# Performance work log

Measured on AMD Instinct MI355X. Metric: run time of the kernel, lower is better.

## Reference

```python
import jax, jax.numpy as jnp
import numpy as np

B, L, D = 2, 2048, 2048
H, KVH, HD, FD = 8, 1, 256, 64   # heads, kv heads, head_dim, feature_dim
CHUNK = 64


def setup_inputs() -> dict:
    key = jax.random.key(0)
    ks = jax.random.split(key, 8)
    hidden_states = jax.random.normal(ks[0], (B, L, D), dtype=jnp.float32)
    # Gemma-style RoPE tables over half the head dim
    half = HD // 2
    inv_freq = 1.0 / (10000.0 ** (jnp.arange(half, dtype=jnp.float32) / half))
    ang = jnp.arange(L, dtype=jnp.float32)[:, None] * inv_freq[None, :]  # [L, half]
    freqs_cos, freqs_sin = jnp.cos(ang), jnp.sin(ang)
    mask = jnp.ones((1, 1, L, L), dtype=bool)  # unused in linear path
    s = 0.02
    Wq = jax.random.normal(ks[1], (D, H * HD), dtype=jnp.float32) * s
    Wk = jax.random.normal(ks[2], (D, KVH * HD), dtype=jnp.float32) * s
    Wv = jax.random.normal(ks[3], (D, KVH * HD), dtype=jnp.float32) * s
    Wo = jax.random.normal(ks[4], (H * HD, D), dtype=jnp.float32) * s
    fmq = jax.random.normal(ks[5], (H, HD, FD), dtype=jnp.float32) * s
    fmk = jax.random.normal(ks[6], (H, HD, FD), dtype=jnp.float32) * s
    return dict(hidden_states=hidden_states, freqs_cos=freqs_cos, freqs_sin=freqs_sin,
                mask=mask, Wq=Wq, Wk=Wk, Wv=Wv, Wo=Wo, fmq=fmq, fmk=fmk)


def _rope(x, cos, sin):
    # x: [B, L, h, HD]; Gemma complex RoPE: first half = real, second half = imag
    half = x.shape[-1] // 2
    x1, x2 = x[..., :half], x[..., half:]
    c = cos[None, :, None, :]
    s = sin[None, :, None, :]
    return jnp.concatenate([x1 * c - x2 * s, x1 * s + x2 * c], axis=-1)


def _hedgehog(x, W):
    # x: [B, H, L, HD], W: [H, HD, FD] -> softmax over cat([xW, -xW]) -> [B,H,L,2*FD]
    p = jnp.einsum('bhld,hdf->bhlf', x, W)
    return jax.nn.softmax(jnp.concatenate([p, -p], axis=-1), axis=-1)


def _chunk_linear_attn(q, k, v, chunk=CHUNK):
    # q,k: [B,H,L,F]; v: [B,H,L,HD]; chunked causal linear attention
    b, h, l, f = q.shape
    dv = v.shape[-1]
    n = l // chunk
    q = q.reshape(b, h, n, chunk, f) * (f ** -0.5)
    k = k.reshape(b, h, n, chunk, f)
    v = v.reshape(b, h, n, chunk, dv)
    kv = jnp.einsum('bhncf,bhncd->bhnfd', k, v)            # per-chunk KV
    kv = jnp.cumsum(kv, axis=2)
    kv = jnp.concatenate([jnp.zeros_like(kv[:, :, :1]), kv[:, :, :-1]], axis=2)  # exclusive prefix
    inter = jnp.einsum('bhncf,bhnfd->bhncd', q, kv)        # cross-chunk term
    s = jnp.einsum('bhnif,bhnjf->bhnij', q, k)             # intra-chunk scores
    tri = jnp.tril(jnp.ones((chunk, chunk), dtype=bool))
    s = jnp.where(tri, s, 0.0)
    intra = jnp.einsum('bhnij,bhnjd->bhnid', s, v)
    return (inter + intra).reshape(b, h, l, dv)


def reference(hidden_states, freqs_cos, freqs_sin, mask, Wq, Wk, Wv, Wo, fmq, fmk):
    b, l, _ = hidden_states.shape
    q = (hidden_states @ Wq).reshape(b, l, H, HD)
    k = (hidden_states @ Wk).reshape(b, l, KVH, HD)
    v = (hidden_states @ Wv).reshape(b, l, KVH, HD)
    q = _rope(q, freqs_cos, freqs_sin)
    k = _rope(k, freqs_cos, freqs_sin)
    # repeat_interleave kv heads to num_heads (MQA expansion)
    rep = H // KVH
    k = jnp.repeat(k, rep, axis=2)
    v = jnp.repeat(v, rep, axis=2)
    q = jnp.transpose(q, (0, 2, 1, 3))  # [B,H,L,HD]
    k = jnp.transpose(k, (0, 2, 1, 3))
    v = jnp.transpose(v, (0, 2, 1, 3))
    q = _hedgehog(q, fmq)
    k = _hedgehog(k, fmk)
    o = _chunk_linear_attn(q, k, v)                         # [B,H,L,HD]
    o = jnp.transpose(o, (0, 2, 1, 3)).reshape(b, l, H * HD)
    return o @ Wo
```

## Files before the change

kernel.cpp:

```cpp
#include <hip/hip_runtime.h>

#define B_ 2
#define L_ 2048
#define D_ 2048
#define H_ 8
#define HD_ 256
#define FD_ 64
#define F_ 128
#define NC_ 32
#define M_ (B_*L_)
#define SCALE_Q 0.08838834764831845f

typedef unsigned short u16;
typedef __attribute__((ext_vector_type(8))) short bf16x8;
typedef __attribute__((ext_vector_type(8))) unsigned short u16x8;
typedef __attribute__((ext_vector_type(4))) unsigned short u16x4;
typedef __attribute__((ext_vector_type(16))) float f32x16;
typedef __attribute__((ext_vector_type(4))) unsigned int u32x4;

#define FMA4(a_, s_, v_) { (a_).x += (s_)*(v_).x; (a_).y += (s_)*(v_).y; \
                           (a_).z += (s_)*(v_).z; (a_).w += (s_)*(v_).w; }


__device__ __forceinline__ u16 bf16_rne(float x) {
  unsigned u = __float_as_uint(x);
  return (u16)((u + 0x7fffu + ((u >> 16) & 1u)) >> 16);
}
__device__ __forceinline__ void bf16_split(float x, u16& h, u16& l) {
  unsigned u = __float_as_uint(x);
  unsigned hb = (u + 0x7fffu + ((u >> 16) & 1u)) >> 16;
  h = (u16)hb;
  float hf = __uint_as_float(hb << 16);
  l = bf16_rne(x - hf);
}

__device__ __forceinline__ void gl_lds16(const u16* g, u16* l) {
  __builtin_amdgcn_global_load_lds(
      (const __attribute__((address_space(1))) unsigned int*)g,
      (__attribute__((address_space(3))) unsigned int*)l, 16, 0, 0);
}

__device__ __forceinline__ size_t kvb_off(int d, int f) {
  return (size_t)(((d >> 7) & 1) * 16384 + ((f >> 5) & 3) * 4096 +
                  ((d >> 6) & 1) * 2048 + ((f >> 4) & 1) * 1024 +
                  ((d >> 5) & 1) * 512 + ((f >> 3) & 1) * 256 +
                  (d & 31) * 8 + (f & 7));
}
__device__ __forceinline__ size_t vb_off(int d, int j) {
  return (size_t)(((d >> 7) & 1) * 8192 + ((j >> 5) & 1) * 4096 +
                  ((d >> 6) & 1) * 2048 + ((j >> 4) & 1) * 1024 +
                  ((d >> 5) & 1) * 512 + ((j >> 3) & 1) * 256 +
                  (d & 31) * 8 + (j & 7));
}

__device__ __forceinline__ void wtrans_body(const float* __restrict__ W, int Nsrc,
                                            int n0, u16* __restrict__ dst,
                                            int P, int kt) {
  int t = threadIdx.x;
  int nn = t & 127, kh = t >> 7;
  const float* src = W + (size_t)(kt * 32 + kh * 16) * Nsrc + n0 + nn;
  u16x8 u0, u1;
  #pragma unroll
  for (int kk = 0; kk < 8; ++kk) u0[kk] = bf16_rne(src[(size_t)kk * Nsrc]);
  #pragma unroll
  for (int kk = 0; kk < 8; ++kk) u1[kk] = bf16_rne(src[(size_t)(kk + 8) * Nsrc]);
  size_t base = ((size_t)P * 64 + kt) * 4096 + (size_t)((nn >> 6) & 1) * 2048
              + (size_t)kh * 1024 + (size_t)((nn >> 5) & 1) * 512
              + (size_t)(nn & 31) * 8;
  *(u16x8*)(dst + base) = u0;
  *(u16x8*)(dst + base + 256) = u1;
}

__global__ __launch_bounds__(256)
void prep_kernel(const float* __restrict__ hs,
                 const float* __restrict__ Wq, const float* __restrict__ Wk,
                 const float* __restrict__ Wv, const float* __restrict__ Wo,
                 const float* __restrict__ fmq, const float* __restrict__ fmk,
                 u16* __restrict__ hsHt, u16* __restrict__ hsLt,
                 u16* __restrict__ WTh, u16* __restrict__ WoTh,
                 u16* __restrict__ fmbtH, u16* __restrict__ fmbtL) {
  int bid = blockIdx.x;
  if (bid < 4096) {
    int gid = bid * 256 + threadIdx.x;
    int r = gid >> 8, u = gid & 255;
    const float* src = hs + (size_t)r * 2048 + u * 8;
    float4 v0 = *(const float4*)src, v1 = *(const float4*)(src + 4);
    float vals[8] = {v0.x, v0.y, v0.z, v0.w, v1.x, v1.y, v1.z, v1.w};
    u16x8 hv, lv;
    #pragma unroll
    for (int j = 0; j < 8; ++j) { u16 hh, ll; bf16_split(vals[j], hh, ll); hv[j] = hh; lv[j] = ll; }
    size_t off = ((size_t)(r >> 6) * 64 + (u >> 2)) * 2048
               + (size_t)((u >> 1) & 1) * 1024 + (size_t)((r >> 5) & 1) * 512
               + (size_t)(u & 1) * 256 + (size_t)(r & 31) * 8;
    *(u16x8*)(hsHt + off) = hv;
    *(u16x8*)(hsLt + off) = lv;
  } else if (bid < 5376) {
    int idx = bid - 4096;
    int P = idx >> 6, kt = idx & 63;
    const float* W; int Nsrc, n0;
    if (P < 16)      { W = Wq; Nsrc = 2048; n0 = P * 128; }
    else if (P < 18) { W = Wk; Nsrc = 256;  n0 = (P - 16) * 128; }
    else             { W = Wv; Nsrc = 256;  n0 = (P - 18) * 128; }
    wtrans_body(W, Nsrc, n0, WTh, P, kt);
  } else if (bid < 5504) {
    int idx = bid - 5376;
    int h16 = idx >> 3, kt = idx & 7;
    const float* src = (h16 < 8) ? (fmq + (size_t)h16 * 16384)
                                 : (fmk + (size_t)(h16 - 8) * 16384);
    int t = threadIdx.x;
    int f = t & 63, kq = t >> 6;
    u16x8 hv, lv;
    #pragma unroll
    for (int i = 0; i < 8; ++i) {
      float val = src[(size_t)(kt * 32 + kq * 8 + i) * 64 + f];
      u16 hh, ll; bf16_split(val, hh, ll); hv[i] = hh; lv[i] = ll;
    }
    size_t base = (size_t)(h16 * 8 + kt) * 2048 + (size_t)(kq >> 1) * 1024
                + (size_t)(f >> 5) * 512 + (size_t)(kq & 1) * 256
                + (size_t)(f & 31) * 8;
    *(u16x8*)(fmbtH + base) = hv;
    *(u16x8*)(fmbtL + base) = lv;
  } else {
    int idx = bid - 5504;
    wtrans_body(Wo, 2048, (idx >> 6) * 128, WoTh, idx >> 6, idx & 63);
  }
}

__global__ __launch_bounds__(256)
void wtrans_wo(const float* __restrict__ Wo, u16* __restrict__ WoTh) {
  wtrans_body(Wo, 2048, blockIdx.x * 128, WoTh, blockIdx.x, blockIdx.y);
}

__global__ __launch_bounds__(256)
void prep_v(const float* __restrict__ v, u16* __restrict__ vbH,
            u16* __restrict__ vbL) {
  int bn = blockIdx.x;
  const float* vp = v + (size_t)bn * 64 * HD_;
  size_t cbout = (size_t)bn * 16384;
  int d = threadIdx.x;
  #pragma unroll
  for (int it = 0; it < 8; ++it) {
    int j0 = it * 8;
    u16x8 hv, lv;
    #pragma unroll
    for (int c = 0; c < 8; ++c) {
      u16 hh, ll; bf16_split(vp[(size_t)(j0 + c) * HD_ + d], hh, ll);
      hv[c] = hh; lv[c] = ll;
    }
    size_t off = cbout + vb_off(d, j0);
    *(u16x8*)(vbH + off) = hv;
    *(u16x8*)(vbL + off) = lv;
  }
}

__device__ __forceinline__ void mfma_body(
    const u16* __restrict__ AtH, const u16* __restrict__ AtL,
    const u16* __restrict__ Bt, float* __restrict__ C, int cstride,
    int bm, int bn) {
  __shared__ __align__(16) u16 AsH[2048];
  __shared__ __align__(16) u16 AsL[2048];
  __shared__ __align__(16) u16 Bs[4096];
  const int t = threadIdx.x, lane = t & 63, wv = t >> 6;
  const u16* aSrc = (wv ? AtL : AtH) + (size_t)bm * 131072 + lane * 8;
  const u16* bSrc = Bt + (size_t)bn * 262144 + wv * 2048 + lane * 8;
  u16* aDst = wv ? AsL : AsH;
  u16* bDst = Bs + wv * 2048;

  f32x16 acc[2][2];
  #pragma unroll
  for (int a = 0; a < 2; ++a)
    #pragma unroll
    for (int b2 = 0; b2 < 2; ++b2)
      #pragma unroll
      for (int r = 0; r < 16; ++r) acc[a][b2][r] = 0.f;

  for (int kt = 0; kt < 64; ++kt) {
    const u16* ak = aSrc + (size_t)kt * 2048;
    const u16* bk = bSrc + (size_t)kt * 4096;
    __syncthreads();
    #pragma unroll
    for (int c = 0; c < 4; ++c) {
      gl_lds16(ak + c * 512, aDst + c * 512);
      gl_lds16(bk + c * 512, bDst + c * 512);
    }
    __syncthreads();

    #pragma unroll
    for (int ks = 0; ks < 2; ++ks) {
      const u16* ph = AsH + ks * 1024 + lane * 8;
      const u16* pl = AsL + ks * 1024 + lane * 8;
      const u16* pb = Bs + wv * 2048 + ks * 1024 + lane * 8;
      bf16x8 a0 = *(const bf16x8*)ph;
      bf16x8 a1 = *(const bf16x8*)(ph + 512);
      bf16x8 b0 = *(const bf16x8*)pb;
      bf16x8 b1 = *(const bf16x8*)(pb + 512);
      acc[0][0] = __builtin_amdgcn_mfma_f32_32x32x16_bf16(a0, b0, acc[0][0], 0, 0, 0);
      acc[0][1] = __builtin_amdgcn_mfma_f32_32x32x16_bf16(a0, b1, acc[0][1], 0, 0, 0);
      acc[1][0] = __builtin_amdgcn_mfma_f32_32x32x16_bf16(a1, b0, acc[1][0], 0, 0, 0);
      acc[1][1] = __builtin_amdgcn_mfma_f32_32x32x16_bf16(a1, b1, acc[1][1], 0, 0, 0);
      bf16x8 l0 = *(const bf16x8*)pl;
      bf16x8 l1 = *(const bf16x8*)(pl + 512);
      acc[0][0] = __builtin_amdgcn_mfma_f32_32x32x16_bf16(l0, b0, acc[0][0], 0, 0, 0);
      acc[0][1] = __builtin_amdgcn_mfma_f32_32x32x16_bf16(l0, b1, acc[0][1], 0, 0, 0);
      acc[1][0] = __builtin_amdgcn_mfma_f32_32x32x16_bf16(l1, b0, acc[1][0], 0, 0, 0);
      acc[1][1] = __builtin_amdgcn_mfma_f32_32x32x16_bf16(l1, b1, acc[1][1], 0, 0, 0);
    }
  }

  const int fr = lane & 31, g = lane >> 5;
  float* Cp = C + (size_t)(bm * 64) * cstride + wv * 64;
  #pragma unroll
  for (int mt = 0; mt < 2; ++mt)
    #pragma unroll
    for (int nt = 0; nt < 2; ++nt) {
      #pragma unroll
      for (int r = 0; r < 16; ++r) {
        int row = mt * 32 + (r & 3) + 8 * (r >> 2) + 4 * g;
        Cp[(size_t)row * cstride + nt * 32 + fr] = acc[mt][nt][r];
      }
    }
}

#define SUB_ 12288
#define MFB(a_, b_, c_) (c_) = __builtin_amdgcn_mfma_f32_32x32x16_bf16((a_), (b_), (c_), 0, 0, 0)

__device__ __forceinline__ void mfma_big_body(
    const u16* __restrict__ AtH, const u16* __restrict__ AtL,
    const u16* __restrict__ Bt, float* __restrict__ C, int cstride,
    int bm, int bn) {
  __shared__ __align__(16) u16 lds[3 * SUB_];
  const int t = threadIdx.x, lane = t & 63, wv = t >> 6;
  const int wm = wv >> 1, wn = wv & 1;

  const u16* gs[6];
  unsigned lo[6], gst[6];
  #pragma unroll
  for (int j = 0; j < 6; ++j) {
    int line = wv * 6 + j;
    if (line < 8) {
      gs[j] = AtH + ((size_t)(2 * bm + (line >> 2)) * 64) * 2048
                  + (size_t)(line & 3) * 512 + lane * 8;
      gst[j] = 2048;
    } else if (line < 16) {
      int l2 = line - 8;
      gs[j] = AtL + ((size_t)(2 * bm + (l2 >> 2)) * 64) * 2048
                  + (size_t)(l2 & 3) * 512 + lane * 8;
      gst[j] = 2048;
    } else {
      int l3 = line - 16;
      gs[j] = Bt + (size_t)bn * 262144 + (size_t)l3 * 512 + lane * 8;
      gst[j] = 4096;
    }
    lo[j] = line * 512;
  }

  f32x16 acc[2][2];
  #pragma unroll
  for (int a = 0; a < 2; ++a)
    #pragma unroll
    for (int b2 = 0; b2 < 2; ++b2)
      #pragma unroll
      for (int r = 0; r < 16; ++r) acc[a][b2][r] = 0.f;

  #pragma unroll
  for (int j = 0; j < 6; ++j) gl_lds16(gs[j], lds + lo[j]);
  #pragma unroll
  for (int j = 0; j < 6; ++j) gl_lds16(gs[j] + gst[j], lds + SUB_ + lo[j]);
  asm volatile("s_waitcnt vmcnt(6)" ::: "memory");
  __builtin_amdgcn_s_barrier();
  __builtin_amdgcn_sched_barrier(0);

  int cb = 0;
  for (int kt = 0; kt < 64; ++kt) {
    int sb = cb + 2 * SUB_; if (sb >= 3 * SUB_) sb -= 3 * SUB_;
    const u16* base = lds + cb;
    const u16* ph0 = base + wm * 2048 + lane * 8;
    const u16* pb0 = base + 8192 + wn * 2048 + lane * 8;

    bf16x8 a0 = *(const bf16x8*)(ph0);
    bf16x8 a1 = *(const bf16x8*)(ph0 + 512);
    bf16x8 l0 = *(const bf16x8*)(ph0 + 4096);
    bf16x8 l1 = *(const bf16x8*)(ph0 + 4608);
    bf16x8 b0 = *(const bf16x8*)(pb0);
    bf16x8 b1 = *(const bf16x8*)(pb0 + 512);
    if (kt < 62) {
      gl_lds16(gs[0] + (size_t)(kt + 2) * gst[0], lds + sb + lo[0]);
      gl_lds16(gs[1] + (size_t)(kt + 2) * gst[1], lds + sb + lo[1]);
      gl_lds16(gs[2] + (size_t)(kt + 2) * gst[2], lds + sb + lo[2]);
    }
    __builtin_amdgcn_s_barrier();
    asm volatile("s_waitcnt lgkmcnt(0)" ::: "memory");
    __builtin_amdgcn_sched_barrier(0);
    __builtin_amdgcn_s_setprio(1);
    MFB(a0, b0, acc[0][0]); MFB(a0, b1, acc[0][1]);
    MFB(a1, b0, acc[1][0]); MFB(a1, b1, acc[1][1]);
    MFB(l0, b0, acc[0][0]); MFB(l0, b1, acc[0][1]);
    MFB(l1, b0, acc[1][0]); MFB(l1, b1, acc[1][1]);
    __builtin_amdgcn_s_setprio(0);
    __builtin_amdgcn_s_barrier();
    __builtin_amdgcn_sched_barrier(0);

    bf16x8 c0 = *(const bf16x8*)(ph0 + 1024);
    bf16x8 c1 = *(const bf16x8*)(ph0 + 1536);
    bf16x8 m0 = *(const bf16x8*)(ph0 + 5120);
    bf16x8 m1 = *(const bf16x8*)(ph0 + 5632);
    bf16x8 d0 = *(const bf16x8*)(pb0 + 1024);
    bf16x8 d1 = *(const bf16x8*)(pb0 + 1536);
    if (kt < 62) {
      gl_lds16(gs[3] + (size_t)(kt + 2) * gst[3], lds + sb + lo[3]);
      gl_lds16(gs[4] + (size_t)(kt + 2) * gst[4], lds + sb + lo[4]);
      gl_lds16(gs[5] + (size_t)(kt + 2) * gst[5], lds + sb + lo[5]);
    }
    __builtin_amdgcn_s_barrier();
    asm volatile("s_waitcnt lgkmcnt(0)" ::: "memory");
    __builtin_amdgcn_sched_barrier(0);
    __builtin_amdgcn_s_setprio(1);
    MFB(c0, d0, acc[0][0]); MFB(c0, d1, acc[0][1]);
    MFB(c1, d0, acc[1][0]); MFB(c1, d1, acc[1][1]);
    MFB(m0, d0, acc[0][0]); MFB(m0, d1, acc[0][1]);
    MFB(m1, d0, acc[1][0]); MFB(m1, d1, acc[1][1]);
    __builtin_amdgcn_s_setprio(0);
    if (kt < 62) asm volatile("s_waitcnt vmcnt(6)" ::: "memory");
    else         asm volatile("s_waitcnt vmcnt(0)" ::: "memory");
    __builtin_amdgcn_s_barrier();
    __builtin_amdgcn_sched_barrier(0);
    cb += SUB_; if (cb == 3 * SUB_) cb = 0;
  }

  const int fr = lane & 31, g = lane >> 5;
  float* Cp = C + (size_t)(bm * 128 + wm * 64) * cstride + wn * 64;
  #pragma unroll
  for (int mt = 0; mt < 2; ++mt)
    #pragma unroll
    for (int nt = 0; nt < 2; ++nt) {
      #pragma unroll
      for (int r = 0; r < 16; ++r) {
        int row = mt * 32 + (r & 3) + 8 * (r >> 2) + 4 * g;
        Cp[(size_t)row * cstride + nt * 32 + fr] = acc[mt][nt][r];
      }
    }
}

__global__ __launch_bounds__(256, 2)
void mfma_q(const u16* __restrict__ hsHt, const u16* __restrict__ hsLt,
            const u16* __restrict__ WTh, float* __restrict__ q) {
  mfma_big_body(hsHt, hsLt, WTh, q + blockIdx.x * 128, 2048,
                blockIdx.y, blockIdx.x);
}

__global__ __launch_bounds__(128, 4)
void mfma_kv(const u16* __restrict__ hsHt, const u16* __restrict__ hsLt,
             const u16* __restrict__ WTh,
             float* __restrict__ k, float* __restrict__ v) {
  int bn = blockIdx.x;
  float* Cb; int co;
  if (bn < 2) { Cb = k; co = bn * 128; }
  else        { Cb = v; co = (bn - 2) * 128; }
  mfma_body(hsHt, hsLt, WTh, Cb + co, 256, blockIdx.y, 16 + bn);
}

__global__ __launch_bounds__(256, 2)
void mfma_wo(const u16* __restrict__ oHt, const u16* __restrict__ oLt,
             const u16* __restrict__ WoTh, float* __restrict__ out) {
  mfma_big_body(oHt, oLt, WoTh, out + blockIdx.x * 128, 2048,
                blockIdx.y, blockIdx.x);
}

__global__ __launch_bounds__(256, 1)
void mfma_hh(const float* __restrict__ q, const float* __restrict__ kx,
             const float* __restrict__ cosb, const float* __restrict__ sinb,
             const u16* __restrict__ fmbtH, const u16* __restrict__ fmbtL,
             float* __restrict__ qf, float* __restrict__ kf,
             const float* __restrict__ vsrc,
             u16* __restrict__ vbH, u16* __restrict__ vbL) {
  int bid = blockIdx.x;
  if (bid >= 512) {
    int bn = bid - 512;
    const float* vp = vsrc + (size_t)bn * 64 * HD_;
    size_t cbout = (size_t)bn * 16384;
    int d = threadIdx.x;
    #pragma unroll
    for (int it = 0; it < 8; ++it) {
      int j0 = it * 8;
      u16x8 hv, lv;
      #pragma unroll
      for (int c = 0; c < 8; ++c) {
        u16 hh, ll; bf16_split(vp[(size_t)(j0 + c) * HD_ + d], hh, ll);
        hv[c] = hh; lv[c] = ll;
      }
      size_t off = cbout + vb_off(d, j0);
      *(u16x8*)(vbH + off) = hv;
      *(u16x8*)(vbL + off) = lv;
    }
    return;
  }
  __shared__ __align__(16) u16 xlds[65536];
  const int t = threadIdx.x;
  const int rt = bid & 31, h16 = bid >> 5;
  const int rowbase = rt * 128;
  const float* xsrc; size_t xstr;
  if (h16 < 8) { xsrc = q + (size_t)h16 * 256; xstr = 2048; }
  else         { xsrc = kx;                    xstr = 256; }

  for (int iter = 0; iter < 16; ++iter) {
    int flat = iter * 1024 + t * 4;
    int r = flat >> 7, dd = flat & 127;
    int grow = rowbase + r;
    int l = grow & 2047;
    const float* xr = xsrc + (size_t)grow * xstr + dd;
    float4 x1 = *(const float4*)xr;
    float4 x2 = *(const float4*)(xr + 128);
    float4 c  = *(const float4*)(cosb + (size_t)l * 128 + dd);
    float4 s  = *(const float4*)(sinb + (size_t)l * 128 + dd);
    float lo4[4] = {x1.x*c.x - x2.x*s.x, x1.y*c.y - x2.y*s.y,
                    x1.z*c.z - x2.z*s.z, x1.w*c.w - x2.w*s.w};
    float hi4[4] = {x1.x*s.x + x2.x*c.x, x1.y*s.y + x2.y*c.y,
                    x1.z*s.z + x2.z*c.z, x1.w*s.w + x2.w*c.w};
    int rt32 = r >> 5, r5 = r & 31;
    #pragma unroll
    for (int half = 0; half < 2; ++half) {
      int d = dd + half * 128;
      int kt = d >> 5, k = d & 31;
      unsigned base = (unsigned)((kt * 4 + rt32) * 2) * 1024
                    + (unsigned)(k >> 4) * 512 + (unsigned)((k >> 3) & 1) * 256
                    + (unsigned)r5 * 8 + (unsigned)(k & 7);
      const float* vv = half ? hi4 : lo4;
      u16x4 hv, lv;
      #pragma unroll
      for (int j = 0; j < 4; ++j) {
        u16 hh, ll; bf16_split(vv[j], hh, ll); hv[j] = hh; lv[j] = ll;
      }
      *(u16x4*)(xlds + base) = hv;
      *(u16x4*)(xlds + 1024 + base) = lv;
    }
  }
  __syncthreads();

  const int w = t >> 6, lane = t & 63;
  f32x16 acc[2];
  #pragma unroll
  for (int nt = 0; nt < 2; ++nt)
    #pragma unroll
    for (int r = 0; r < 16; ++r) acc[nt][r] = 0.f;

  const u16* fmbH = fmbtH + (size_t)h16 * 8 * 2048;
  const u16* fmbL = fmbtL + (size_t)h16 * 8 * 2048;
  #pragma unroll
  for (int kt = 0; kt < 8; ++kt) {
    unsigned xb = (unsigned)((kt * 4 + w) * 2) * 1024;
    #pragma unroll
    for (int ks = 0; ks < 2; ++ks) {
      bf16x8 xh = *(const bf16x8*)(xlds + xb + ks * 512 + lane * 8);
      bf16x8 xl = *(const bf16x8*)(xlds + xb + 1024 + ks * 512 + lane * 8);
      #pragma unroll
      for (int nt = 0; nt < 2; ++nt) {
        size_t fb = (size_t)kt * 2048 + ks * 1024 + nt * 512 + lane * 8;
        bf16x8 bh_ = *(const bf16x8*)((const short*)(fmbH + fb));
        bf16x8 bl_ = *(const bf16x8*)((const short*)(fmbL + fb));
        MFB(xh, bh_, acc[nt]); MFB(xl, bh_, acc[nt]); MFB(xh, bl_, acc[nt]);
      }
    }
  }

  const int g = lane >> 5, f31 = lane & 31;
  float* outp = (h16 < 8) ? qf : kf;
  const int hh = h16 & 7;
  #pragma unroll
  for (int r = 0; r < 16; ++r) {
    int rowl = (r & 3) + 8 * (r >> 2) + 4 * g;
    int grow = rowbase + w * 32 + rowl;
    float p0 = acc[0][r], p1 = acc[1][r];
    float m = fmaxf(fabsf(p0), fabsf(p1));
    #pragma unroll
    for (int off = 16; off > 0; off >>= 1) m = fmaxf(m, __shfl_xor(m, off, 64));
    float e0 = __expf(p0 - m),  e0n = __expf(-p0 - m);
    float e1 = __expf(p1 - m),  e1n = __expf(-p1 - m);
    float zl = e0 + e0n + e1 + e1n;
    #pragma unroll
    for (int off = 16; off > 0; off >>= 1) zl += __shfl_xor(zl, off, 64);
    float inv = 1.0f / zl;
    int b = grow >> 11, l = grow & 2047;
    size_t ob = ((size_t)((b * 8 + hh) * 2048 + l)) * 128;
    outp[ob + f31]       = e0 * inv;
    outp[ob + 32 + f31]  = e1 * inv;
    outp[ob + 64 + f31]  = e0n * inv;
    outp[ob + 96 + f31]  = e1n * inv;
  }
}

__global__ __launch_bounds__(256)
void chunk_kv_kernel(const float* __restrict__ kf, const float* __restrict__ v,
                     u16* __restrict__ kvbH, u16* __restrict__ kvbL) {
  __shared__ __align__(16) float kfs[64][128];
  int n = blockIdx.x & (NC_ - 1), bh = blockIdx.x >> 5;
  int b = bh >> 3;
  const float* kfp = kf + ((size_t)bh * L_ + (size_t)n * 64) * F_;
  int t = threadIdx.x;
  #pragma unroll
  for (int it = 0; it < 8; ++it) {
    int flat = t * 4 + it * 1024;
    *(float4*)&kfs[flat >> 7][flat & 127] = *(const float4*)(kfp + flat);
  }
  __syncthreads();
  int dg = t & 63;
  int fg = t >> 6;
  const float* vp = v + (size_t)(b * L_ + n * 64) * HD_ + dg * 4;
  size_t cb = (size_t)blockIdx.x * 32768;
  #pragma unroll
  for (int pass = 0; pass < 4; ++pass) {
    int f0 = fg * 8 + pass * 32;
    float4 acc[8];
    #pragma unroll
    for (int i = 0; i < 8; ++i) acc[i] = make_float4(0.f, 0.f, 0.f, 0.f);
    for (int j = 0; j < 64; ++j) {
      float4 vv = *(const float4*)(vp + (size_t)j * HD_);
      float4 ka = *(const float4*)&kfs[j][f0];
      float4 kb = *(const float4*)&kfs[j][f0 + 4];
      FMA4(acc[0], ka.x, vv); FMA4(acc[1], ka.y, vv);
      FMA4(acc[2], ka.z, vv); FMA4(acc[3], ka.w, vv);
      FMA4(acc[4], kb.x, vv); FMA4(acc[5], kb.y, vv);
      FMA4(acc[6], kb.z, vv); FMA4(acc[7], kb.w, vv);
    }
    #pragma unroll
    for (int c = 0; c < 4; ++c) {
      u16x8 hv, lv;
      #pragma unroll
      for (int ff = 0; ff < 8; ++ff) {
        float xs = (c == 0) ? acc[ff].x : (c == 1) ? acc[ff].y
                 : (c == 2) ? acc[ff].z : acc[ff].w;
        u16 hh, ll; bf16_split(xs, hh, ll); hv[ff] = hh; lv[ff] = ll;
      }
      int d = dg * 4 + c;
      size_t off = cb + kvb_off(d, f0);
      *(u16x8*)(kvbH + off) = hv;
      *(u16x8*)(kvbL + off) = lv;
    }
  }
}

__global__ __launch_bounds__(256)
void chunk_scan_kernel(u16* __restrict__ kvbH, u16* __restrict__ kvbL) {
  int bh = blockIdx.x >> 4, g = blockIdx.x & 15;
  int d = threadIdx.x;
  size_t off = kvb_off(d, g * 8);
  float run[8] = {0.f, 0.f, 0.f, 0.f, 0.f, 0.f, 0.f, 0.f};
  for (int n = 0; n < NC_; ++n) {
    size_t a = ((size_t)(bh * 32 + n)) * 32768 + off;
    u16x8 hv = *(u16x8*)(kvbH + a);
    u16x8 lv = *(u16x8*)(kvbL + a);
    u16x8 oh, ol;
    #pragma unroll
    for (int c = 0; c < 8; ++c) {
      float val = __uint_as_float((unsigned)hv[c] << 16)
                + __uint_as_float((unsigned)lv[c] << 16);
      u16 hh, ll; bf16_split(run[c], hh, ll); oh[c] = hh; ol[c] = ll;
      run[c] += val;
    }
    *(u16x8*)(kvbH + a) = oh;
    *(u16x8*)(kvbL + a) = ol;
  }
}

__global__ __launch_bounds__(256, 2)
void chunk_attn_kernel(const float* __restrict__ qf, const float* __restrict__ kf,
                       const u16* __restrict__ vbH, const u16* __restrict__ vbL,
                       const u16* __restrict__ kvbH, const u16* __restrict__ kvbL,
                       u16* __restrict__ oHt, u16* __restrict__ oLt) {
  __shared__ __align__(16) u16 lds[32768];
  const int n = blockIdx.x & (NC_ - 1), bh = blockIdx.x >> 5;
  const int h = bh & 7, b = bh >> 3;
  const int t = threadIdx.x;
  const int w = t >> 6, i31 = t & 31, G = (t >> 5) & 1;
  const int l8 = (t & 63) * 8;

  {
    const float* qp = qf + ((size_t)bh * L_ + (size_t)n * 64) * F_;
    const float* kp = kf + ((size_t)bh * L_ + (size_t)n * 64) * F_;
    int o8 = t & 15, ib = t >> 4;
    #pragma unroll
    for (int iter = 0; iter < 4; ++iter) {
      int i = ib + iter * 16;
      int it = i >> 5, ks = o8 >> 1;
      int sub = (it * 8 + ks) * 512 + (o8 & 1) * 256 + (i & 31) * 8;
      {
        const float* src = qp + (size_t)i * 128 + o8 * 8;
        float4 a = *(const float4*)src, c = *(const float4*)(src + 4);
        float vals[8] = {a.x, a.y, a.z, a.w, c.x, c.y, c.z, c.w};
        u16x8 hv, lv;
        #pragma unroll
        for (int j = 0; j < 8; ++j) {
          u16 hh, ll; bf16_split(vals[j] * SCALE_Q, hh, ll);
          hv[j] = hh; lv[j] = ll;
        }
        *(u16x8*)(lds + sub) = hv;
        *(u16x8*)(lds + 8192 + sub) = lv;
      }
      {
        const float* src = kp + (size_t)i * 128 + o8 * 8;
        float4 a = *(const float4*)src, c = *(const float4*)(src + 4);
        float vals[8] = {a.x, a.y, a.z, a.w, c.x, c.y, c.z, c.w};
        u16x8 hv, lv;
        #pragma unroll
        for (int j = 0; j < 8; ++j) {
          u16 hh, ll; bf16_split(vals[j], hh, ll);
          hv[j] = hh; lv[j] = ll;
        }
        *(u16x8*)(lds + 16384 + sub) = hv;
        *(u16x8*)(lds + 24576 + sub) = lv;
      }
    }
  }
  __syncthreads();

  const u16* Lq  = lds;
  const u16* Lql = lds + 8192;
  const u16* Lk  = lds + 16384;
  const u16* Lkl = lds + 24576;

  f32x16 st[2][2];
  #pragma unroll
  for (int a = 0; a < 2; ++a)
    #pragma unroll
    for (int c = 0; c < 2; ++c)
      #pragma unroll
      for (int r = 0; r < 16; ++r) st[a][c][r] = 0.f;

  #pragma unroll
  for (int ks = 0; ks < 8; ++ks) {
    bf16x8 kh0 = *(const bf16x8*)(Lk  + ks * 512 + l8);
    bf16x8 kh1 = *(const bf16x8*)(Lk  + (8 + ks) * 512 + l8);
    bf16x8 kl0 = *(const bf16x8*)(Lkl + ks * 512 + l8);
    bf16x8 kl1 = *(const bf16x8*)(Lkl + (8 + ks) * 512 + l8);
    bf16x8 qh0 = *(const bf16x8*)(Lq  + ks * 512 + l8);
    bf16x8 qh1 = *(const bf16x8*)(Lq  + (8 + ks) * 512 + l8);
    bf16x8 ql0 = *(const bf16x8*)(Lql + ks * 512 + l8);
    bf16x8 ql1 = *(const bf16x8*)(Lql + (8 + ks) * 512 + l8);
    MFB(kh0, qh0, st[0][0]); MFB(kh0, ql0, st[0][0]); MFB(kl0, qh0, st[0][0]);
    MFB(kh0, qh1, st[0][1]); MFB(kh0, ql1, st[0][1]); MFB(kl0, qh1, st[0][1]);
    MFB(kh1, qh0, st[1][0]); MFB(kh1, ql0, st[1][0]); MFB(kl1, qh0, st[1][0]);
    MFB(kh1, qh1, st[1][1]); MFB(kh1, ql1, st[1][1]); MFB(kl1, qh1, st[1][1]);
  }

// ... 62 lines not shown

  {
    size_t cb = (size_t)blockIdx.x * 32768;
    #pragma unroll
    for (int ks = 0; ks < 8; ++ks) {
      bf16x8 qa_h0 = *(const bf16x8*)(Lq  + ks * 512 + l8);
      bf16x8 qa_h1 = *(const bf16x8*)(Lq  + (8 + ks) * 512 + l8);
      bf16x8 qa_l0 = *(const bf16x8*)(Lql + ks * 512 + l8);
      bf16x8 qa_l1 = *(const bf16x8*)(Lql + (8 + ks) * 512 + l8);
      #pragma unroll
      for (int nt = 0; nt < 2; ++nt) {
        size_t base = cb + kvb_off(w * 64 + nt * 32, ks * 16) + l8;
        bf16x8 kvH = *(const bf16x8*)((const short*)(kvbH + base));
        bf16x8 kvL = *(const bf16x8*)((const short*)(kvbL + base));
        MFB(qa_h0, kvH, acc[0][nt]); MFB(qa_l0, kvH, acc[0][nt]);
        MFB(qa_h0, kvL, acc[0][nt]);
        MFB(qa_h1, kvH, acc[1][nt]); MFB(qa_l1, kvH, acc[1][nt]);
        MFB(qa_h1, kvL, acc[1][nt]);
      }
    }
  }

  {
    int p = b * NC_ + n;
    #pragma unroll
    for (int mt = 0; mt < 2; ++mt)
      #pragma unroll
      for (int nt = 0; nt < 2; ++nt) {
        int u_ = h * 32 + w * 8 + nt * 4 + (i31 >> 3);
        size_t ob = ((size_t)p * 64 + (u_ >> 2)) * 2048
                  + (size_t)((u_ >> 1) & 1) * 1024 + (size_t)mt * 512
                  + (size_t)(u_ & 1) * 256 + (size_t)(i31 & 7);
        #pragma unroll
        for (int r = 0; r < 16; ++r) {
          int rr = (r & 3) + 8 * (r >> 2) + 4 * G;
          u16 hh, ll; bf16_split(acc[mt][nt][r], hh, ll);
          oHt[ob + (size_t)rr * 8] = hh;
          oLt[ob + (size_t)rr * 8] = ll;
        }
      }
  }
}

extern "C" void kernel_launch(void* const* d_in, const int* in_sizes, int n_in,
                              void* d_out, int out_size, void* d_ws, size_t ws_size,
                              hipStream_t stream) {
  const float* hs   = (const float*)d_in[0];
  const float* fcos = (const float*)d_in[1];
  const float* fsin = (const float*)d_in[2];
  const float* Wq  = (const float*)d_in[4];
  const float* Wk  = (const float*)d_in[5];
  const float* Wv  = (const float*)d_in[6];
  const float* Wo  = (const float*)d_in[7];
  const float* fmq = (const float*)d_in[8];
  const float* fmk = (const float*)d_in[9];
  float* out = (float*)d_out;

  float* ws = (float*)d_ws;
  float* q  = ws;
  float* k  = q  + (size_t)M_ * 2048;
  float* v  = k  + (size_t)M_ * 256;
  float* qf = v  + (size_t)M_ * 256;
  float* kf = qf + (size_t)B_ * H_ * L_ * F_;
  float* kvr = kf + (size_t)B_ * H_ * L_ * F_;

  u16* hsHt = (u16*)kvr;
  u16* hsLt = hsHt + (size_t)M_ * 2048;
  u16* WTh  = hsLt + (size_t)M_ * 2048;
  u16* fmbtH = WTh + (size_t)1280 * 4096;
  u16* fmbtL = fmbtH + (size_t)131072 * 2;
  u16* kvbH = (u16*)kvr;
  u16* kvbL = kvbH + (size_t)512 * 32768;
  u16* oHt  = (u16*)q;
  u16* oLt  = oHt + (size_t)M_ * 2048;

  const size_t WS_BASE = (size_t)142606336;
  bool bigws = ws_size >= WS_BASE + (size_t)12582912;
  u16* WoTh = bigws ? (u16*)((char*)d_ws + WS_BASE) : (u16*)kvr;
  u16* vbH  = bigws ? (u16*)((char*)d_ws + WS_BASE + 8388608) : (u16*)k;
  u16* vbL  = vbH + (size_t)64 * 16384;

  prep_kernel<<<bigws ? 6528 : 5504, 256, 0, stream>>>(
      hs, Wq, Wk, Wv, Wo, fmq, fmk, hsHt, hsLt, WTh, WoTh, fmbtH, fmbtL);
  mfma_q<<<dim3(16, 32), 256, 0, stream>>>(hsHt, hsLt, WTh, q);
  mfma_kv<<<dim3(4, 64), 128, 0, stream>>>(hsHt, hsLt, WTh, k, v);
  mfma_hh<<<bigws ? 576 : 512, 256, 0, stream>>>(
      q, k, fcos, fsin, fmbtH, fmbtL, qf, kf, v, vbH, vbL);
  if (!bigws)
    prep_v<<<B_ * NC_, 256, 0, stream>>>(v, vbH, vbL);
  chunk_kv_kernel<<<B_ * H_ * NC_, 256, 0, stream>>>(kf, v, kvbH, kvbL);
  chunk_scan_kernel<<<256, 256, 0, stream>>>(kvbH, kvbL);
  chunk_attn_kernel<<<B_ * H_ * NC_, 256, 0, stream>>>(qf, kf, vbH, vbL,
                                                       kvbH, kvbL, oHt, oLt);
  if (!bigws)
    wtrans_wo<<<dim3(16, 64), 256, 0, stream>>>(Wo, WoTh);
  mfma_wo<<<dim3(16, 32), 256, 0, stream>>>(oHt, oLt, WoTh, out);
}
```

Baseline: 481.2 us.

## Merge Q and KV projections into one launch and fuse chunk KV with scan

The separate Q and K/V projection GEMMs become a single mfma_qkv launch that uses the big 128x128 tile body for all 20 column blocks. The per-chunk KV outer-product kernel and the prefix-scan kernel are fused into one kernel that keeps a running KV sum in registers, so per-chunk KV partials are no longer written and read back. The cost is that the fused scan runs only 256 blocks sequentially over 32 chunks, doing scalar FMAs per thread, which cuts parallelism compared with the 512-block chunk_kv kernel.

Result: slower. 500.1 us (+3.9%).

```diff
diff --git a/kernel.cpp b/kernel.cpp
--- a/kernel.cpp
+++ b/kernel.cpp
@@ -17,9 +17,6 @@
 typedef __attribute__((ext_vector_type(4))) unsigned short u16x4;
 typedef __attribute__((ext_vector_type(16))) float f32x16;
 typedef __attribute__((ext_vector_type(4))) unsigned int u32x4;
-
-#define FMA4(a_, s_, v_) { (a_).x += (s_)*(v_).x; (a_).y += (s_)*(v_).y; \
-                           (a_).z += (s_)*(v_).z; (a_).w += (s_)*(v_).w; }
 
 
 __device__ __forceinline__ u16 bf16_rne(float x) {
@@ -153,74 +150,6 @@
   }
 }
 
-__device__ __forceinline__ void mfma_body(
-    const u16* __restrict__ AtH, const u16* __restrict__ AtL,
-    const u16* __restrict__ Bt, float* __restrict__ C, int cstride,
-    int bm, int bn) {
-  __shared__ __align__(16) u16 AsH[2048];
-  __shared__ __align__(16) u16 AsL[2048];
-  __shared__ __align__(16) u16 Bs[4096];
-  const int t = threadIdx.x, lane = t & 63, wv = t >> 6;
-  const u16* aSrc = (wv ? AtL : AtH) + (size_t)bm * 131072 + lane * 8;
-  const u16* bSrc = Bt + (size_t)bn * 262144 + wv * 2048 + lane * 8;
-  u16* aDst = wv ? AsL : AsH;
-  u16* bDst = Bs + wv * 2048;
-
-  f32x16 acc[2][2];
-  #pragma unroll
-  for (int a = 0; a < 2; ++a)
-    #pragma unroll
-    for (int b2 = 0; b2 < 2; ++b2)
-      #pragma unroll
-      for (int r = 0; r < 16; ++r) acc[a][b2][r] = 0.f;
-
-  for (int kt = 0; kt < 64; ++kt) {
-    const u16* ak = aSrc + (size_t)kt * 2048;
-    const u16* bk = bSrc + (size_t)kt * 4096;
-    __syncthreads();
-    #pragma unroll
-    for (int c = 0; c < 4; ++c) {
-      gl_lds16(ak + c * 512, aDst + c * 512);
-      gl_lds16(bk + c * 512, bDst + c * 512);
-    }
-    __syncthreads();
-
-    #pragma unroll
-    for (int ks = 0; ks < 2; ++ks) {
-      const u16* ph = AsH + ks * 1024 + lane * 8;
-      const u16* pl = AsL + ks * 1024 + lane * 8;
-      const u16* pb = Bs + wv * 2048 + ks * 1024 + lane * 8;
-      bf16x8 a0 = *(const bf16x8*)ph;
-      bf16x8 a1 = *(const bf16x8*)(ph + 512);
-      bf16x8 b0 = *(const bf16x8*)pb;
-      bf16x8 b1 = *(const bf16x8*)(pb + 512);
-      acc[0][0] = __builtin_amdgcn_mfma_f32_32x32x16_bf16(a0, b0, acc[0][0], 0, 0, 0);
-      acc[0][1] = __builtin_amdgcn_mfma_f32_32x32x16_bf16(a0, b1, acc[0][1], 0, 0, 0);
-      acc[1][0] = __builtin_amdgcn_mfma_f32_32x32x16_bf16(a1, b0, acc[1][0], 0, 0, 0);
-      acc[1][1] = __builtin_amdgcn_mfma_f32_32x32x16_bf16(a1, b1, acc[1][1], 0, 0, 0);
-      bf16x8 l0 = *(const bf16x8*)pl;
-      bf16x8 l1 = *(const bf16x8*)(pl + 512);
-      acc[0][0] = __builtin_amdgcn_mfma_f32_32x32x16_bf16(l0, b0, acc[0][0], 0, 0, 0);
-      acc[0][1] = __builtin_amdgcn_mfma_f32_32x32x16_bf16(l0, b1, acc[0][1], 0, 0, 0);
-      acc[1][0] = __builtin_amdgcn_mfma_f32_32x32x16_bf16(l1, b0, acc[1][0], 0, 0, 0);
-      acc[1][1] = __builtin_amdgcn_mfma_f32_32x32x16_bf16(l1, b1, acc[1][1], 0, 0, 0);
-    }
-  }
-
-  const int fr = lane & 31, g = lane >> 5;
-  float* Cp = C + (size_t)(bm * 64) * cstride + wv * 64;
-  #pragma unroll
-  for (int mt = 0; mt < 2; ++mt)
-    #pragma unroll
-    for (int nt = 0; nt < 2; ++nt) {
-      #pragma unroll
-      for (int r = 0; r < 16; ++r) {
-        int row = mt * 32 + (r & 3) + 8 * (r >> 2) + 4 * g;
-        Cp[(size_t)row * cstride + nt * 32 + fr] = acc[mt][nt][r];
-      }
-    }
-}
-
 #define SUB_ 12288
 #define MFB(a_, b_, c_) (c_) = __builtin_amdgcn_mfma_f32_32x32x16_bf16((a_), (b_), (c_), 0, 0, 0)
 
@@ -342,21 +271,16 @@
 }
 
 __global__ __launch_bounds__(256, 2)
-void mfma_q(const u16* __restrict__ hsHt, const u16* __restrict__ hsLt,
-            const u16* __restrict__ WTh, float* __restrict__ q) {
-  mfma_big_body(hsHt, hsLt, WTh, q + blockIdx.x * 128, 2048,
-                blockIdx.y, blockIdx.x);
-}
-
-__global__ __launch_bounds__(128, 4)
-void mfma_kv(const u16* __restrict__ hsHt, const u16* __restrict__ hsLt,
-             const u16* __restrict__ WTh,
-             float* __restrict__ k, float* __restrict__ v) {
+void mfma_qkv(const u16* __restrict__ hsHt, const u16* __restrict__ hsLt,
+              const u16* __restrict__ WTh,
+              float* __restrict__ q, float* __restrict__ k,
+              float* __restrict__ v) {
   int bn = blockIdx.x;
-  float* Cb; int co;
-  if (bn < 2) { Cb = k; co = bn * 128; }
-  else        { Cb = v; co = (bn - 2) * 128; }
-  mfma_body(hsHt, hsLt, WTh, Cb + co, 256, blockIdx.y, 16 + bn);
+  float* Cb; int cs, co;
+  if (bn < 16)      { Cb = q; cs = 2048; co = bn * 128; }
+  else if (bn < 18) { Cb = k; cs = 256;  co = (bn - 16) * 128; }
+  else              { Cb = v; cs = 256;  co = (bn - 18) * 128; }
+  mfma_big_body(hsHt, hsLt, WTh, Cb + co, cs, blockIdx.y, bn);
 }
 
 __global__ __launch_bounds__(256, 2)
@@ -489,75 +413,40 @@
 }
 
 __global__ __launch_bounds__(256)
-void chunk_kv_kernel(const float* __restrict__ kf, const float* __restrict__ v,
-                     u16* __restrict__ kvbH, u16* __restrict__ kvbL) {
-  __shared__ __align__(16) float kfs[64][128];
-  int n = blockIdx.x & (NC_ - 1), bh = blockIdx.x >> 5;
+void chunk_kvscan_kernel(const float* __restrict__ kf, const float* __restrict__ v,
+                         u16* __restrict__ kvbH, u16* __restrict__ kvbL) {
+  __shared__ __align__(16) float kfs[64][8];
+  int bh = blockIdx.x >> 4, g = blockIdx.x & 15;
   int b = bh >> 3;
-  const float* kfp = kf + ((size_t)bh * L_ + (size_t)n * 64) * F_;
-  int t = threadIdx.x;
-  #pragma unroll
-  for (int it = 0; it < 8; ++it) {
-    int flat = t * 4 + it * 1024;
-    *(float4*)&kfs[flat >> 7][flat & 127] = *(const float4*)(kfp + flat);
-  }
-  __syncthreads();
-  int dg = t & 63;
-  int fg = t >> 6;
-  const float* vp = v + (size_t)(b * L_ + n * 64) * HD_ + dg * 4;
-  size_t cb = (size_t)blockIdx.x * 32768;
-  #pragma unroll
-  for (int pass = 0; pass < 4; ++pass) {
-    int f0 = fg * 8 + pass * 32;
-    float4 acc[8];
-    #pragma unroll
-    for (int i = 0; i < 8; ++i) acc[i] = make_float4(0.f, 0.f, 0.f, 0.f);
-    for (int j = 0; j < 64; ++j) {
-      float4 vv = *(const float4*)(vp + (size_t)j * HD_);
-      float4 ka = *(const float4*)&kfs[j][f0];
-      float4 kb = *(const float4*)&kfs[j][f0 + 4];
-      FMA4(acc[0], ka.x, vv); FMA4(acc[1], ka.y, vv);
-      FMA4(acc[2], ka.z, vv); FMA4(acc[3], ka.w, vv);
-      FMA4(acc[4], kb.x, vv); FMA4(acc[5], kb.y, vv);
-      FMA4(acc[6], kb.z, vv); FMA4(acc[7], kb.w, vv);
-    }
-    #pragma unroll
-    for (int c = 0; c < 4; ++c) {
-      u16x8 hv, lv;
-      #pragma unroll
-      for (int ff = 0; ff < 8; ++ff) {
-        float xs = (c == 0) ? acc[ff].x : (c == 1) ? acc[ff].y
-                 : (c == 2) ? acc[ff].z : acc[ff].w;
-        u16 hh, ll; bf16_split(xs, hh, ll); hv[ff] = hh; lv[ff] = ll;
-      }
-      int d = dg * 4 + c;
-      size_t off = cb + kvb_off(d, f0);
-      *(u16x8*)(kvbH + off) = hv;
-      *(u16x8*)(kvbL + off) = lv;
-    }
-  }
-}
-
-__global__ __launch_bounds__(256)
-void chunk_scan_kernel(u16* __restrict__ kvbH, u16* __restrict__ kvbL) {
-  int bh = blockIdx.x >> 4, g = blockIdx.x & 15;
+  int f0 = g * 8;
   int d = threadIdx.x;
-  size_t off = kvb_off(d, g * 8);
+  size_t off = kvb_off(d, f0);
+  const float* kfb = kf + (size_t)bh * L_ * F_ + f0;
+  const float* vb_ = v + (size_t)b * L_ * HD_ + d;
   float run[8] = {0.f, 0.f, 0.f, 0.f, 0.f, 0.f, 0.f, 0.f};
   for (int n = 0; n < NC_; ++n) {
+    u16x8 oh, ol;
+    #pragma unroll
+    for (int c = 0; c < 8; ++c) {
+      u16 hh, ll; bf16_split(run[c], hh, ll); oh[c] = hh; ol[c] = ll;
+    }
     size_t a = ((size_t)(bh * 32 + n)) * 32768 + off;
-    u16x8 hv = *(u16x8*)(kvbH + a);
-    u16x8 lv = *(u16x8*)(kvbL + a);
-    u16x8 oh, ol;
-    #pragma unroll
-    for (int c = 0; c < 8; ++c) {
-      float val = __uint_as_float((unsigned)hv[c] << 16)
-                + __uint_as_float((unsigned)lv[c] << 16);
-      u16 hh, ll; bf16_split(run[c], hh, ll); oh[c] = hh; ol[c] = ll;
-      run[c] += val;
-    }
     *(u16x8*)(kvbH + a) = oh;
     *(u16x8*)(kvbL + a) = ol;
+    __syncthreads();
+    if (threadIdx.x < 128) {
+      int flat = threadIdx.x * 4;
+      int j = flat >> 3, f = flat & 7;
+      *(float4*)&kfs[j][f] =
+          *(const float4*)(kfb + (size_t)(n * 64 + j) * F_ + f);
+    }
+    __syncthreads();
+    const float* vp = vb_ + (size_t)n * 64 * HD_;
+    for (int j = 0; j < 64; ++j) {
+      float vv = vp[(size_t)j * HD_];
+      #pragma unroll
+      for (int c = 0; c < 8; ++c) run[c] += kfs[j][c] * vv;
+    }
   }
 }
 
@@ -786,14 +675,12 @@
 
   prep_kernel<<<bigws ? 6528 : 5504, 256, 0, stream>>>(
       hs, Wq, Wk, Wv, Wo, fmq, fmk, hsHt, hsLt, WTh, WoTh, fmbtH, fmbtL);
-  mfma_q<<<dim3(16, 32), 256, 0, stream>>>(hsHt, hsLt, WTh, q);
-  mfma_kv<<<dim3(4, 64), 128, 0, stream>>>(hsHt, hsLt, WTh, k, v);
+  mfma_qkv<<<dim3(20, 32), 256, 0, stream>>>(hsHt, hsLt, WTh, q, k, v);
   mfma_hh<<<bigws ? 576 : 512, 256, 0, stream>>>(
       q, k, fcos, fsin, fmbtH, fmbtL, qf, kf, v, vbH, vbL);
   if (!bigws)
     prep_v<<<B_ * NC_, 256, 0, stream>>>(v, vbH, vbL);
-  chunk_kv_kernel<<<B_ * H_ * NC_, 256, 0, stream>>>(kf, v, kvbH, kvbL);
-  chunk_scan_kernel<<<256, 256, 0, stream>>>(kvbH, kvbL);
+  chunk_kvscan_kernel<<<16 * 16, 256, 0, stream>>>(kf, v, kvbH, kvbL);
   chunk_attn_kernel<<<B_ * H_ * NC_, 256, 0, stream>>>(qf, kf, vbH, vbL,
                                                        kvbH, kvbL, oHt, oLt);
   if (!bigws)
```

## Fuse per-chunk KV outer product with exclusive prefix scan in one kernel

Applied to the files above, without the earlier changes.

Replaces the separate chunk_kv and chunk_scan kernels with a single kernel in which each block owns an (batch-head, 8-feature) slice and walks the chunks sequentially, accumulating K^T V in registers and writing the exclusive prefix as split bf16 hi/lo. This removes the round trip of per-chunk KV through global memory and one kernel launch. In exchange, parallelism drops to 256 blocks that each run a serial 32-chunk loop with scalar FMAs, two barriers per chunk and small LDS staging. Total work also becomes more serialized.

New measurement: 504.6 us. 1.05x slower.

```diff
diff --git a/kernel.cpp b/kernel.cpp
--- a/kernel.cpp
+++ b/kernel.cpp
@@ -17,9 +17,6 @@
 typedef __attribute__((ext_vector_type(4))) unsigned short u16x4;
 typedef __attribute__((ext_vector_type(16))) float f32x16;
 typedef __attribute__((ext_vector_type(4))) unsigned int u32x4;
-
-#define FMA4(a_, s_, v_) { (a_).x += (s_)*(v_).x; (a_).y += (s_)*(v_).y; \
-                           (a_).z += (s_)*(v_).z; (a_).w += (s_)*(v_).w; }
 
 
 __device__ __forceinline__ u16 bf16_rne(float x) {
@@ -489,75 +486,40 @@
 }
 
 __global__ __launch_bounds__(256)
-void chunk_kv_kernel(const float* __restrict__ kf, const float* __restrict__ v,
-                     u16* __restrict__ kvbH, u16* __restrict__ kvbL) {
-  __shared__ __align__(16) float kfs[64][128];
-  int n = blockIdx.x & (NC_ - 1), bh = blockIdx.x >> 5;
+void chunk_kvscan_kernel(const float* __restrict__ kf, const float* __restrict__ v,
+                         u16* __restrict__ kvbH, u16* __restrict__ kvbL) {
+  __shared__ __align__(16) float kfs[64][8];
+  int bh = blockIdx.x >> 4, g = blockIdx.x & 15;
   int b = bh >> 3;
-  const float* kfp = kf + ((size_t)bh * L_ + (size_t)n * 64) * F_;
-  int t = threadIdx.x;
-  #pragma unroll
-  for (int it = 0; it < 8; ++it) {
-    int flat = t * 4 + it * 1024;
-    *(float4*)&kfs[flat >> 7][flat & 127] = *(const float4*)(kfp + flat);
-  }
-  __syncthreads();
-  int dg = t & 63;
-  int fg = t >> 6;
-  const float* vp = v + (size_t)(b * L_ + n * 64) * HD_ + dg * 4;
-  size_t cb = (size_t)blockIdx.x * 32768;
-  #pragma unroll
-  for (int pass = 0; pass < 4; ++pass) {
-    int f0 = fg * 8 + pass * 32;
-    float4 acc[8];
-    #pragma unroll
-    for (int i = 0; i < 8; ++i) acc[i] = make_float4(0.f, 0.f, 0.f, 0.f);
-    for (int j = 0; j < 64; ++j) {
-      float4 vv = *(const float4*)(vp + (size_t)j * HD_);
-      float4 ka = *(const float4*)&kfs[j][f0];
-      float4 kb = *(const float4*)&kfs[j][f0 + 4];
-      FMA4(acc[0], ka.x, vv); FMA4(acc[1], ka.y, vv);
-      FMA4(acc[2], ka.z, vv); FMA4(acc[3], ka.w, vv);
-      FMA4(acc[4], kb.x, vv); FMA4(acc[5], kb.y, vv);
-      FMA4(acc[6], kb.z, vv); FMA4(acc[7], kb.w, vv);
-    }
-    #pragma unroll
-    for (int c = 0; c < 4; ++c) {
-      u16x8 hv, lv;
-      #pragma unroll
-      for (int ff = 0; ff < 8; ++ff) {
-        float xs = (c == 0) ? acc[ff].x : (c == 1) ? acc[ff].y
-                 : (c == 2) ? acc[ff].z : acc[ff].w;
-        u16 hh, ll; bf16_split(xs, hh, ll); hv[ff] = hh; lv[ff] = ll;
-      }
-      int d = dg * 4 + c;
-      size_t off = cb + kvb_off(d, f0);
-      *(u16x8*)(kvbH + off) = hv;
-      *(u16x8*)(kvbL + off) = lv;
-    }
-  }
-}
-
-__global__ __launch_bounds__(256)
-void chunk_scan_kernel(u16* __restrict__ kvbH, u16* __restrict__ kvbL) {
-  int bh = blockIdx.x >> 4, g = blockIdx.x & 15;
+  int f0 = g * 8;
   int d = threadIdx.x;
-  size_t off = kvb_off(d, g * 8);
+  size_t off = kvb_off(d, f0);
+  const float* kfb = kf + (size_t)bh * L_ * F_ + f0;
+  const float* vb_ = v + (size_t)b * L_ * HD_ + d;
   float run[8] = {0.f, 0.f, 0.f, 0.f, 0.f, 0.f, 0.f, 0.f};
   for (int n = 0; n < NC_; ++n) {
+    u16x8 oh, ol;
+    #pragma unroll
+    for (int c = 0; c < 8; ++c) {
+      u16 hh, ll; bf16_split(run[c], hh, ll); oh[c] = hh; ol[c] = ll;
+    }
     size_t a = ((size_t)(bh * 32 + n)) * 32768 + off;
-    u16x8 hv = *(u16x8*)(kvbH + a);
-    u16x8 lv = *(u16x8*)(kvbL + a);
-    u16x8 oh, ol;
-    #pragma unroll
-    for (int c = 0; c < 8; ++c) {
-      float val = __uint_as_float((unsigned)hv[c] << 16)
-                + __uint_as_float((unsigned)lv[c] << 16);
-      u16 hh, ll; bf16_split(run[c], hh, ll); oh[c] = hh; ol[c] = ll;
-      run[c] += val;
-    }
     *(u16x8*)(kvbH + a) = oh;
     *(u16x8*)(kvbL + a) = ol;
+    __syncthreads();
+    if (threadIdx.x < 128) {
+      int flat = threadIdx.x * 4;
+      int j = flat >> 3, f = flat & 7;
+      *(float4*)&kfs[j][f] =
+          *(const float4*)(kfb + (size_t)(n * 64 + j) * F_ + f);
+    }
+    __syncthreads();
+    const float* vp = vb_ + (size_t)n * 64 * HD_;
+    for (int j = 0; j < 64; ++j) {
+      float vv = vp[(size_t)j * HD_];
+      #pragma unroll
+      for (int c = 0; c < 8; ++c) run[c] += kfs[j][c] * vv;
+    }
   }
 }
 
@@ -792,8 +754,7 @@
       q, k, fcos, fsin, fmbtH, fmbtL, qf, kf, v, vbH, vbL);
   if (!bigws)
     prep_v<<<B_ * NC_, 256, 0, stream>>>(v, vbH, vbL);
-  chunk_kv_kernel<<<B_ * H_ * NC_, 256, 0, stream>>>(kf, v, kvbH, kvbL);
-  chunk_scan_kernel<<<256, 256, 0, stream>>>(kvbH, kvbL);
+  chunk_kvscan_kernel<<<16 * 16, 256, 0, stream>>>(kf, v, kvbH, kvbL);
   chunk_attn_kernel<<<B_ * H_ * NC_, 256, 0, stream>>>(qf, kf, vbH, vbL,
                                                        kvbH, kvbL, oHt, oLt);
   if (!bigws)
```

## Compute per-chunk KV outer products with split-bf16 MFMA instead of FP32 FMAs

Applied to the files above, without the earlier changes.

Replaces the scalar FP32 FMA chunk_kv kernel with an MFMA version. kf is converted to hi/lo bf16 pairs in an MFMA-friendly LDS layout, and the pre-split bf16 V buffers (vbH/vbL) are used as the B operand, with three MFMAs per step approximating FP32 precision. Results are exchanged across lane halves so each half writes either the high or the low bf16 part. The aim is to cut the ALU cost of this stage, in exchange for a small precision change and a dependence on vbH/vbL already being ready.

Measured after the change: 466.1 us. 1.03x faster.

```diff
diff --git a/kernel.cpp b/kernel.cpp
--- a/kernel.cpp
+++ b/kernel.cpp
@@ -17,9 +17,6 @@
 typedef __attribute__((ext_vector_type(4))) unsigned short u16x4;
 typedef __attribute__((ext_vector_type(16))) float f32x16;
 typedef __attribute__((ext_vector_type(4))) unsigned int u32x4;
-
-#define FMA4(a_, s_, v_) { (a_).x += (s_)*(v_).x; (a_).y += (s_)*(v_).y; \
-                           (a_).z += (s_)*(v_).z; (a_).w += (s_)*(v_).w; }
 
 
 __device__ __forceinline__ u16 bf16_rne(float x) {
@@ -488,52 +485,74 @@
   }
 }
 
-__global__ __launch_bounds__(256)
-void chunk_kv_kernel(const float* __restrict__ kf, const float* __restrict__ v,
-                     u16* __restrict__ kvbH, u16* __restrict__ kvbL) {
-  __shared__ __align__(16) float kfs[64][128];
-  int n = blockIdx.x & (NC_ - 1), bh = blockIdx.x >> 5;
-  int b = bh >> 3;
-  const float* kfp = kf + ((size_t)bh * L_ + (size_t)n * 64) * F_;
-  int t = threadIdx.x;
-  #pragma unroll
-  for (int it = 0; it < 8; ++it) {
-    int flat = t * 4 + it * 1024;
-    *(float4*)&kfs[flat >> 7][flat & 127] = *(const float4*)(kfp + flat);
+__global__ __launch_bounds__(256, 2)
+void chunk_kv_mfma(const float* __restrict__ kf,
+                   const u16* __restrict__ vbH, const u16* __restrict__ vbL,
+                   u16* __restrict__ kvbH, u16* __restrict__ kvbL) {
+  __shared__ __align__(16) u16 kfA[16384];
+  const int n = blockIdx.x & (NC_ - 1), bh = blockIdx.x >> 5;
+  const int b = bh >> 3;
+  const int t = threadIdx.x;
+
+  {
+    const float* kfp = kf + ((size_t)bh * L_ + (size_t)n * 64) * F_;
+    int f = t & 127, jb = (t >> 7) * 32;
+    int ft = f >> 5, frow = f & 31;
+    #pragma unroll
+    for (int jj = 0; jj < 32; ++jj) {
+      int j = jb + jj;
+      float val = kfp[(size_t)j * F_ + f];
+      u16 hh, ll; bf16_split(val, hh, ll);
+      int idx = ft * 2048 + (j >> 4) * 512 + ((j >> 3) & 1) * 256
+              + frow * 8 + (j & 7);
+      kfA[idx] = hh;
+      kfA[8192 + idx] = ll;
+    }
   }
   __syncthreads();
-  int dg = t & 63;
-  int fg = t >> 6;
-  const float* vp = v + (size_t)(b * L_ + n * 64) * HD_ + dg * 4;
+
+  const int w = t >> 6, lane = t & 63, g = lane >> 5, d31 = lane & 31;
+  size_t vcb = ((size_t)(b * NC_ + n)) * 16384;
   size_t cb = (size_t)blockIdx.x * 32768;
-  #pragma unroll
-  for (int pass = 0; pass < 4; ++pass) {
-    int f0 = fg * 8 + pass * 32;
-    float4 acc[8];
-    #pragma unroll
-    for (int i = 0; i < 8; ++i) acc[i] = make_float4(0.f, 0.f, 0.f, 0.f);
-    for (int j = 0; j < 64; ++j) {
-      float4 vv = *(const float4*)(vp + (size_t)j * HD_);
-      float4 ka = *(const float4*)&kfs[j][f0];
-      float4 kb = *(const float4*)&kfs[j][f0 + 4];
-      FMA4(acc[0], ka.x, vv); FMA4(acc[1], ka.y, vv);
-      FMA4(acc[2], ka.z, vv); FMA4(acc[3], ka.w, vv);
-      FMA4(acc[4], kb.x, vv); FMA4(acc[5], kb.y, vv);
-      FMA4(acc[6], kb.z, vv); FMA4(acc[7], kb.w, vv);
-    }
-    #pragma unroll
-    for (int c = 0; c < 4; ++c) {
+
+  bf16x8 ah[4], al[4];
+  #pragma unroll
+  for (int ks = 0; ks < 4; ++ks) {
+    ah[ks] = *(const bf16x8*)(kfA + w * 2048 + ks * 512 + lane * 8);
+    al[ks] = *(const bf16x8*)(kfA + 8192 + w * 2048 + ks * 512 + lane * 8);
+  }
+
+  #pragma unroll
+  for (int dt = 0; dt < 8; ++dt) {
+    f32x16 acc;
+    #pragma unroll
+    for (int r = 0; r < 16; ++r) acc[r] = 0.f;
+    #pragma unroll
+    for (int ks = 0; ks < 4; ++ks) {
+      size_t bv = vcb + vb_off(dt * 32, ks * 16) + lane * 8;
+      bf16x8 bhv = *(const bf16x8*)((const short*)(vbH + bv));
+      bf16x8 blv = *(const bf16x8*)((const short*)(vbL + bv));
+      MFB(ah[ks], bhv, acc); MFB(al[ks], bhv, acc); MFB(ah[ks], blv, acc);
+    }
+    int d = dt * 32 + d31;
+    #pragma unroll
+    for (int qd = 0; qd < 4; ++qd) {
+      float vals[8];
+      #pragma unroll
+      for (int c = 0; c < 4; ++c) {
+        float mine = acc[qd * 4 + c];
+        float other = __shfl_xor(mine, 32, 64);
+        vals[c]     = g ? other : mine;
+        vals[c + 4] = g ? mine : other;
+      }
       u16x8 hv, lv;
       #pragma unroll
-      for (int ff = 0; ff < 8; ++ff) {
-        float xs = (c == 0) ? acc[ff].x : (c == 1) ? acc[ff].y
-                 : (c == 2) ? acc[ff].z : acc[ff].w;
-        u16 hh, ll; bf16_split(xs, hh, ll); hv[ff] = hh; lv[ff] = ll;
-      }
-      int d = dg * 4 + c;
-      size_t off = cb + kvb_off(d, f0);
-      *(u16x8*)(kvbH + off) = hv;
-      *(u16x8*)(kvbL + off) = lv;
+      for (int c = 0; c < 8; ++c) {
+        u16 hh, ll; bf16_split(vals[c], hh, ll); hv[c] = hh; lv[c] = ll;
+      }
+      size_t off8 = cb + kvb_off(d, w * 32 + qd * 8);
+      if (g == 0) *(u16x8*)(kvbH + off8) = hv;
+      else        *(u16x8*)(kvbL + off8) = lv;
     }
   }
 }
@@ -792,7 +811,7 @@
       q, k, fcos, fsin, fmbtH, fmbtL, qf, kf, v, vbH, vbL);
   if (!bigws)
     prep_v<<<B_ * NC_, 256, 0, stream>>>(v, vbH, vbL);
-  chunk_kv_kernel<<<B_ * H_ * NC_, 256, 0, stream>>>(kf, v, kvbH, kvbL);
+  chunk_kv_mfma<<<B_ * H_ * NC_, 256, 0, stream>>>(kf, vbH, vbL, kvbH, kvbL);
   chunk_scan_kernel<<<256, 256, 0, stream>>>(kvbH, kvbL);
   chunk_attn_kernel<<<B_ * H_ * NC_, 256, 0, stream>>>(qf, kf, vbH, vbL,
                                                        kvbH, kvbL, oHt, oLt);
```
